# Kernel optimization log

Measured on AMD Instinct MI355X. Metric: run time of the kernel, lower is better.

Reference implementation:

```python
import jax, jax.numpy as jnp
import numpy as np

N_HEAD = 16
NEG = 1e10


def setup_inputs() -> dict:
    key = jax.random.key(0)
    k1, k2, k3 = jax.random.split(key, 3)
    nx = 1024
    B, S = 2, 2048
    x = jax.random.normal(k1, (B, S, nx), dtype=jnp.float32)
    w_attn = jax.random.normal(k2, (nx, 3 * nx), dtype=jnp.float32) * (1.0 / np.sqrt(nx))
    b_attn = jnp.zeros((3 * nx,), dtype=jnp.float32)
    w_proj = jax.random.normal(k3, (nx, nx), dtype=jnp.float32) * (1.0 / np.sqrt(nx))
    b_proj = jnp.zeros((nx,), dtype=jnp.float32)
    return {"x": x, "w_attn": w_attn, "b_attn": b_attn, "w_proj": w_proj, "b_proj": b_proj}


def reference(x, w_attn, b_attn, w_proj, b_proj):
    B, S, nx = x.shape
    d = nx // N_HEAD
    qkv = x @ w_attn + b_attn                      # [B,S,3*nx]
    q, k, v = jnp.split(qkv, 3, axis=-1)
    # split heads: [B,S,nx] -> [B,H,S,d]
    q = q.reshape(B, S, N_HEAD, d).transpose(0, 2, 1, 3)
    k = k.reshape(B, S, N_HEAD, d).transpose(0, 2, 1, 3)
    v = v.reshape(B, S, N_HEAD, d).transpose(0, 2, 1, 3)
    # present: stack of (key stored as [B,H,S,d], value) like torch code
    present = jnp.stack((k, v))                    # [2,B,H,S,d]
    # scores with scale and additive causal mask (GPT-2 style: w*b - 1e10*(1-b))
    w = jnp.einsum('bhqd,bhkd->bhqk', q, k) / jnp.sqrt(jnp.float32(d))
    mask = jnp.tril(jnp.ones((S, S), dtype=w.dtype))[None, None]
    w = w * mask - NEG * (1.0 - mask)
    w = jax.nn.softmax(w, axis=-1)
    a = jnp.einsum('bhqk,bhkd->bhqd', w, v)        # [B,H,S,d]
    a = a.transpose(0, 2, 1, 3).reshape(B, S, nx)  # merge heads
    a = a @ w_proj + b_proj
    return (a, present)
```

## Files before the change

### kernel.cpp

```cpp
#include <hip/hip_runtime.h>
#include <stdint.h>
#include <stddef.h>

#define DEVI __device__ __forceinline__

typedef __bf16 bf16x8 __attribute__((ext_vector_type(8)));
typedef float  f32x4  __attribute__((ext_vector_type(4)));
typedef float  f32x16 __attribute__((ext_vector_type(16)));
typedef unsigned short u16;
typedef uint32_t u32;
typedef u16 u16x8 __attribute__((ext_vector_type(8)));
typedef u16 u16x4 __attribute__((ext_vector_type(4)));
typedef u32 u32x2 __attribute__((ext_vector_type(2)));
typedef u32 u32x4 __attribute__((ext_vector_type(4)));

typedef __attribute__((address_space(1))) void as1_void;
typedef __attribute__((address_space(3))) void as3_void;

static constexpr float SC = 0.18033688011112042f;

DEVI u16 f2bf(float f) {
  uint32_t u = __builtin_bit_cast(uint32_t, f);
  u += 0x7fffu + ((u >> 16) & 1u);
  return (u16)(u >> 16);
}

DEVI void gload_lds16(const void* g, void* l) {
  __builtin_amdgcn_global_load_lds((as1_void*)(void*)g, (as3_void*)l, 16, 0, 0);
}

#if __has_builtin(__builtin_amdgcn_exp2f)
DEVI float fast_exp2(float x) { return __builtin_amdgcn_exp2f(x); }
#else
DEVI float fast_exp2(float x) { return exp2f(x); }
#endif

DEVI u32 cvtpk(float lo, float hi) {
  u32 r;
  asm("v_cvt_pk_bf16_f32 %0, %1, %2" : "=v"(r) : "v"(lo), "v"(hi));
  return r;
}
DEVI void plswap(u32& a, u32& b) {
  asm("v_permlane32_swap_b32 %0, %1" : "+v"(a), "+v"(b));
}

__global__ __launch_bounds__(256) void k_cvt(const float* __restrict__ in,
                                             u16* __restrict__ out, int n) {
  int i = (blockIdx.x * 256 + threadIdx.x) * 4;
  if (i >= n) return;
  const float4 v = *(const float4*)(in + i);
  u16x4 o = { f2bf(v.x), f2bf(v.y), f2bf(v.z), f2bf(v.w) };
  *(u16x4*)(out + i) = o;
}

__global__ __launch_bounds__(256) void k_tcvt(const float* __restrict__ in,
                                              u16* __restrict__ out, int R, int C) {
  __shared__ float tile[32][33];
  const int c0 = blockIdx.x * 32, r0 = blockIdx.y * 32;
  const int tx = threadIdx.x, ty = threadIdx.y;
#pragma unroll
  for (int i = ty; i < 32; i += 8)
    tile[i][tx] = in[(size_t)(r0 + i) * C + (c0 + tx)];
  __syncthreads();
#pragma unroll
  for (int i = ty; i < 32; i += 8)
    out[(size_t)(c0 + i) * R + (r0 + tx)] = f2bf(tile[tx][i]);
}

__global__ __launch_bounds__(256) void k_vt(const u16* __restrict__ in,
                                            u16* __restrict__ out) {
  __shared__ u16 tile[64][72];
  const int tid = threadIdx.x;
  const int s0 = blockIdx.x * 64;
  const int bh = blockIdx.y;
  const size_t ib = (size_t)bh * 131072;
#pragma unroll
  for (int it = 0; it < 2; ++it) {
    const int r = (tid >> 3) + it * 32;
    const int c8 = (tid & 7) * 8;
    u16x8 v = *(const u16x8*)(in + ib + (size_t)(s0 + r) * 64 + c8);
    *(u16x8*)&tile[r][c8] = v;
  }
  __syncthreads();
#pragma unroll
  for (int it = 0; it < 2; ++it) {
    const int d = (tid >> 3) + it * 32;
    const int s8 = (tid & 7) * 8;
    u16x8 v;
#pragma unroll
    for (int jj = 0; jj < 8; ++jj) v[jj] = tile[s8 + jj][d];
    *(u16x8*)(out + ib + (size_t)d * 2048 + s0 + s8) = v;
  }
}

template <int EPI>
__global__ __launch_bounds__(256) void k_gemm(
    const u16* __restrict__ A, const u16* __restrict__ Bt,
    const float* __restrict__ bias,
    u16* __restrict__ wq, u16* __restrict__ wk, u16* __restrict__ wv,
    float* __restrict__ pk, float* __restrict__ pv, float* __restrict__ of) {
  constexpr int K = 1024;
  __shared__ __align__(16) u16 Ash[2][128 * 32];
  __shared__ __align__(16) u16 Bsh[2][128 * 32];
  const int tid = threadIdx.x;
  const int lane = tid & 63, wid = tid >> 6;
  const int wm = wid >> 1, wn = wid & 1;
  const int lr = lane & 15, lg = lane >> 4;
  const int m0 = blockIdx.y * 128, n0 = blockIdx.x * 128;

  const int c = wid * 64 + lane;
  const u16* Ag1 = A + (size_t)(m0 + (c >> 2)) * K + (c & 3) * 8;
  const u16* Ag2 = A + (size_t)(m0 + 64 + (c >> 2)) * K + (c & 3) * 8;
  const u16* Bg1 = Bt + (size_t)(n0 + (c >> 2)) * K + (c & 3) * 8;
  const u16* Bg2 = Bt + (size_t)(n0 + 64 + (c >> 2)) * K + (c & 3) * 8;

  f32x4 acc[4][4];
#pragma unroll
  for (int i = 0; i < 4; ++i)
#pragma unroll
    for (int j = 0; j < 4; ++j) acc[i][j] = (f32x4)0.0f;

#define STAGE(sel, kk)                                        \
  {                                                           \
    gload_lds16(Ag1 + (kk), &Ash[sel][wid * 512]);            \
    gload_lds16(Ag2 + (kk), &Ash[sel][2048 + wid * 512]);     \
    gload_lds16(Bg1 + (kk), &Bsh[sel][wid * 512]);            \
    gload_lds16(Bg2 + (kk), &Bsh[sel][2048 + wid * 512]);     \
  }

  STAGE(0, 0)
  __syncthreads();
  int cur = 0;
  for (int k0 = 0; k0 < K; k0 += 32) {
    if (k0 + 32 < K) STAGE(cur ^ 1, k0 + 32)
    bf16x8 af[4], bfr[4];
#pragma unroll
    for (int f = 0; f < 4; ++f) {
      af[f]  = *(const bf16x8*)&Ash[cur][(wm * 64 + f * 16 + lr) * 32 + lg * 8];
      bfr[f] = *(const bf16x8*)&Bsh[cur][(wn * 64 + f * 16 + lr) * 32 + lg * 8];
    }
#pragma unroll
    for (int i = 0; i < 4; ++i)
#pragma unroll
      for (int j = 0; j < 4; ++j)
        acc[i][j] = __builtin_amdgcn_mfma_f32_16x16x32_bf16(af[i], bfr[j], acc[i][j], 0, 0, 0);
    __syncthreads();
    cur ^= 1;
  }
#undef STAGE

  if constexpr (EPI == 0) {
#pragma unroll
    for (int j = 0; j < 4; ++j) {
      const int n = n0 + wn * 64 + j * 16 + lr;
      const float bv = bias[n];
      const int sec = n >> 10;
      const int nn = n & 1023;
      const int h = nn >> 6, dd = nn & 63;
#pragma unroll
      for (int i = 0; i < 4; ++i) {
        const int mb = m0 + wm * 64 + i * 16 + lg * 4;
        const int bb = mb >> 11, ss = mb & 2047;
        const size_t ib = (size_t)(bb * 16 + h) * 131072 + (size_t)ss * 64 + dd;
        if (sec == 0) {
#pragma unroll
          for (int r = 0; r < 4; ++r)
            wq[ib + (size_t)r * 64] = f2bf(acc[i][j][r] + bv);
        } else if (sec == 1) {
#pragma unroll
          for (int r = 0; r < 4; ++r) {
            const float v = acc[i][j][r] + bv;
            wk[ib + (size_t)r * 64] = f2bf(v);
            pk[ib + (size_t)r * 64] = v;
          }
        } else {
#pragma unroll
          for (int r = 0; r < 4; ++r) {
            const float v = acc[i][j][r] + bv;
            wv[ib + (size_t)r * 64] = f2bf(v);
            pv[ib + (size_t)r * 64] = v;
          }
        }
      }
    }
  } else {
#pragma unroll
    for (int j = 0; j < 4; ++j) {
      const int n = n0 + wn * 64 + j * 16 + lr;
      const float bv = bias[n];
#pragma unroll
      for (int i = 0; i < 4; ++i) {
        const int mb = m0 + wm * 64 + i * 16 + lg * 4;
#pragma unroll
        for (int r = 0; r < 4; ++r)
          of[(size_t)(mb + r) * 1024 + n] = acc[i][j][r] + bv;
      }
    }
  }
}

__global__ __launch_bounds__(128) void k_attn(const u16* __restrict__ Q,
                                              const u16* __restrict__ Kp,
                                              const u16* __restrict__ VT,
                                              u16* __restrict__ AO) {
  __shared__ __align__(16) u16 Ksh[3][4096];
  __shared__ __align__(16) u16 Vsh[3][4096];

  const int tid = threadIdx.x;
  const int lane = tid & 63, w = tid >> 6;
  const int l31 = lane & 31, hi = lane >> 5;
  const int bid = blockIdx.x;
  const int bh = bid & 31;
  const int j4 = bid >> 8;
  const int g  = (bid >> 5) & 7;
  const int qt = (j4 == 0) ? (31 - g) : (j4 == 1) ? g : (j4 == 2) ? (23 - g) : (8 + g);
  const int b = bh >> 4, h = bh & 15;
  const size_t hb = (size_t)bh * (2048 * 64);

  const int T = qt + 1;
  const int qb = qt * 64 + w * 32;

  const int srow = w * 32 + (lane >> 3);
  const int sslot = (lane & 7) ^ (lane >> 3);
  const u16* Kg = Kp + hb + (size_t)srow * 64 + sslot * 8;
  const u16* Vg = VT + hb + (size_t)srow * 2048 + sslot * 8;

#define STAGEA(sel, jt)                                                       \
  {                                                                           \
    gload_lds16(Kg + (size_t)(jt) * 4096,          &Ksh[sel][w * 2048]);      \
    gload_lds16(Kg + (size_t)(jt) * 4096 + 512,    &Ksh[sel][w * 2048 + 512]);\
    gload_lds16(Kg + (size_t)(jt) * 4096 + 1024,   &Ksh[sel][w * 2048 + 1024]);\
    gload_lds16(Kg + (size_t)(jt) * 4096 + 1536,   &Ksh[sel][w * 2048 + 1536]);\
    gload_lds16(Vg + (size_t)(jt) * 64,            &Vsh[sel][w * 2048]);      \
    gload_lds16(Vg + (size_t)(jt) * 64 + 16384,    &Vsh[sel][w * 2048 + 512]);\
    gload_lds16(Vg + (size_t)(jt) * 64 + 32768,    &Vsh[sel][w * 2048 + 1024]);\
    gload_lds16(Vg + (size_t)(jt) * 64 + 49152,    &Vsh[sel][w * 2048 + 1536]);\
  }

  const u16* Qp = Q + hb + (size_t)(qb + l31) * 64 + hi * 8;
  const bf16x8 qf0 = *(const bf16x8*)(Qp);
  const bf16x8 qf1 = *(const bf16x8*)(Qp + 16);
  const bf16x8 qf2 = *(const bf16x8*)(Qp + 32);
  const bf16x8 qf3 = *(const bf16x8*)(Qp + 48);

  f32x16 o0 = (f32x16)0.0f, o1 = (f32x16)0.0f;
  float mrun = -1e30f, lrun = 0.0f;

  const int xr = l31 & 7;

  STAGEA(0, 0)
  if (T > 1) {
    STAGEA(1, 1)
    asm volatile("s_waitcnt vmcnt(8)" ::: "memory");
  } else {
    asm volatile("s_waitcnt vmcnt(0)" ::: "memory");
  }
  __builtin_amdgcn_sched_barrier(0);
  __builtin_amdgcn_s_barrier();
  __builtin_amdgcn_sched_barrier(0);

  int cur = 0;
  for (int jt = 0; jt < T; ++jt) {
    const bool pf = (jt + 2 < T);
    int nb = cur + 2; if (nb >= 3) nb -= 3;
    if (pf) STAGEA(nb, jt + 2)
    const u16* Kb = Ksh[cur];
    const u16* Vb = Vsh[cur];
    bf16x8 kf[2][4];
#pragma unroll
    for (int s = 0; s < 2; ++s)
#pragma unroll
      for (int c = 0; c < 4; ++c)
        kf[s][c] = *(const bf16x8*)&Kb[(s * 32 + l31) * 64 + (((2 * c + hi) ^ xr) * 8)];

    f32x16 s0 = (f32x16)0.0f, s1 = (f32x16)0.0f;
    __builtin_amdgcn_s_setprio(1);
    s0 = __builtin_amdgcn_mfma_f32_32x32x16_bf16(kf[0][0], qf0, s0, 0, 0, 0);
    s1 = __builtin_amdgcn_mfma_f32_32x32x16_bf16(kf[1][0], qf0, s1, 0, 0, 0);
    s0 = __builtin_amdgcn_mfma_f32_32x32x16_bf16(kf[0][1], qf1, s0, 0, 0, 0);
    s1 = __builtin_amdgcn_mfma_f32_32x32x16_bf16(kf[1][1], qf1, s1, 0, 0, 0);
    s0 = __builtin_amdgcn_mfma_f32_32x32x16_bf16(kf[0][2], qf2, s0, 0, 0, 0);
    s1 = __builtin_amdgcn_mfma_f32_32x32x16_bf16(kf[1][2], qf2, s1, 0, 0, 0);
    s0 = __builtin_amdgcn_mfma_f32_32x32x16_bf16(kf[0][3], qf3, s0, 0, 0, 0);
    s1 = __builtin_amdgcn_mfma_f32_32x32x16_bf16(kf[1][3], qf3, s1, 0, 0, 0);
    __builtin_amdgcn_s_setprio(0);

    if (jt == T - 1) {
      const int qrel = w * 32 + l31;
      const int h4 = hi * 4;
#pragma unroll
      for (int r = 0; r < 16; ++r) {
        const int kp = (r & 3) + ((r >> 2) << 3) + h4;
        s0[r] = (kp <= qrel) ? s0[r] : -1e30f;
        s1[r] = (kp + 32 <= qrel) ? s1[r] : -1e30f;
      }
    }

    float t8[8];
#pragma unroll
    for (int r = 0; r < 8; ++r)
      t8[r] = fmaxf(fmaxf(s0[r], s0[r + 8]), fmaxf(s1[r], s1[r + 8]));
    float tm = fmaxf(fmaxf(fmaxf(t8[0], t8[1]), fmaxf(t8[2], t8[3])),
                     fmaxf(fmaxf(t8[4], t8[5]), fmaxf(t8[6], t8[7])));
    tm = fmaxf(tm, __shfl_xor(tm, 32));
    if (!__all(tm <= mrun)) {
      const float mnew = fmaxf(mrun, tm);
      const float al = fast_exp2((mrun - mnew) * SC);
      mrun = mnew;
      lrun *= al;
#pragma unroll
      for (int r = 0; r < 16; ++r) { o0[r] *= al; o1[r] *= al; }
    }
    const float nb2 = -mrun * SC;
#pragma unroll
    for (int r = 0; r < 16; ++r) {
      s0[r] = fast_exp2(fmaf(s0[r], SC, nb2));
      s1[r] = fast_exp2(fmaf(s1[r], SC, nb2));
    }
    float u8[8];
#pragma unroll
    for (int r = 0; r < 8; ++r)
      u8[r] = (s0[r] + s0[r + 8]) + (s1[r] + s1[r + 8]);
    lrun += ((u8[0] + u8[1]) + (u8[2] + u8[3])) + ((u8[4] + u8[5]) + (u8[6] + u8[7]));

    bf16x8 pb0, pb1, pb2, pb3;
#define PACK_CHUNK(sv, bb, dst)                                   \
    {                                                             \
      u32 a0 = cvtpk(sv[bb + 0], sv[bb + 1]);                     \
      u32 a1 = cvtpk(sv[bb + 2], sv[bb + 3]);                     \
      u32 a2 = cvtpk(sv[bb + 4], sv[bb + 5]);                     \
      u32 a3 = cvtpk(sv[bb + 6], sv[bb + 7]);                     \
      plswap(a0, a2);                                             \
      plswap(a1, a3);                                             \
      u32x4 fv = {a0, a1, a2, a3};                                \
      dst = __builtin_bit_cast(bf16x8, fv);                       \
    }
    PACK_CHUNK(s0, 0, pb0)
    PACK_CHUNK(s0, 8, pb1)
    PACK_CHUNK(s1, 0, pb2)
    PACK_CHUNK(s1, 8, pb3)
#undef PACK_CHUNK

    bf16x8 vf[2][4];
#pragma unroll
    for (int mt = 0; mt < 2; ++mt)
#pragma unroll
      for (int c = 0; c < 4; ++c)
        vf[mt][c] = *(const bf16x8*)&Vb[(mt * 32 + l31) * 64 + (((2 * c + hi) ^ xr) * 8)];

    __builtin_amdgcn_s_setprio(1);
    o0 = __builtin_amdgcn_mfma_f32_32x32x16_bf16(vf[0][0], pb0, o0, 0, 0, 0);
    o1 = __builtin_amdgcn_mfma_f32_32x32x16_bf16(vf[1][0], pb0, o1, 0, 0, 0);
    o0 = __builtin_amdgcn_mfma_f32_32x32x16_bf16(vf[0][1], pb1, o0, 0, 0, 0);
    o1 = __builtin_amdgcn_mfma_f32_32x32x16_bf16(vf[1][1], pb1, o1, 0, 0, 0);
    o0 = __builtin_amdgcn_mfma_f32_32x32x16_bf16(vf[0][2], pb2, o0, 0, 0, 0);
    o1 = __builtin_amdgcn_mfma_f32_32x32x16_bf16(vf[1][2], pb2, o1, 0, 0, 0);
    o0 = __builtin_amdgcn_mfma_f32_32x32x16_bf16(vf[0][3], pb3, o0, 0, 0, 0);
    o1 = __builtin_amdgcn_mfma_f32_32x32x16_bf16(vf[1][3], pb3, o1, 0, 0, 0);
    __builtin_amdgcn_s_setprio(0);

    if (pf) asm volatile("s_waitcnt vmcnt(8)" ::: "memory");
    else    asm volatile("s_waitcnt vmcnt(0)" ::: "memory");
    __builtin_amdgcn_sched_barrier(0);
    __builtin_amdgcn_s_barrier();
    __builtin_amdgcn_sched_barrier(0);
    cur = (cur + 1 == 3) ? 0 : cur + 1;
  }
#undef STAGEA

  const float lt = lrun + __shfl_xor(lrun, 32);
  const float inv = 1.0f / lt;
  u16* aorow = AO + (size_t)(b * 2048 + qb + l31) * 1024 + h * 64 + hi * 4;
#pragma unroll
  for (int g2 = 0; g2 < 4; ++g2) {
    u32 w0 = cvtpk(o0[4 * g2 + 0] * inv, o0[4 * g2 + 1] * inv);
    u32 w1 = cvtpk(o0[4 * g2 + 2] * inv, o0[4 * g2 + 3] * inv);
    u32x2 ww = {w0, w1};
    *(u32x2*)(aorow + g2 * 8) = ww;
  }
#pragma unroll
  for (int g2 = 0; g2 < 4; ++g2) {
    u32 w0 = cvtpk(o1[4 * g2 + 0] * inv, o1[4 * g2 + 1] * inv);
    u32 w1 = cvtpk(o1[4 * g2 + 2] * inv, o1[4 * g2 + 3] * inv);
    u32x2 ww = {w0, w1};
    *(u32x2*)(aorow + 32 + g2 * 8) = ww;
  }
}

extern "C" void kernel_launch(void* const* d_in, const int* in_sizes, int n_in,
                              void* d_out, int out_size, void* d_ws, size_t ws_size,
                              hipStream_t stream) {
  const float* x      = (const float*)d_in[0];
  const float* w_attn = (const float*)d_in[1];
  const float* b_attn = (const float*)d_in[2];
  const float* w_proj = (const float*)d_in[3];
  const float* b_proj = (const float*)d_in[4];
  float* out = (float*)d_out;

  char* ws = (char*)d_ws;
  u16* x_bf  = (u16*)(ws);
  u16* wat_t = (u16*)(ws + 8388608);
  u16* wpj_t = (u16*)(ws + 14680064);
  u16* q_ws  = (u16*)(ws + 16777216);
  u16* k_ws  = (u16*)(ws + 25165824);
  u16* v_ws  = (u16*)(ws + 33554432);
  u16* a_ws  = (u16*)(ws + 41943040);
  u16* vT_ws = (u16*)(ws);

  k_cvt<<<4096, 256, 0, stream>>>(x, x_bf, 4194304);
  k_tcvt<<<dim3(96, 32), dim3(32, 8), 0, stream>>>(w_attn, wat_t, 1024, 3072);
  k_tcvt<<<dim3(32, 32), dim3(32, 8), 0, stream>>>(w_proj, wpj_t, 1024, 1024);

  k_gemm<0><<<dim3(24, 32), 256, 0, stream>>>(x_bf, wat_t, b_attn,
                                              q_ws, k_ws, v_ws,
                                              out + 4194304, out + 8388608, nullptr);

  k_vt<<<dim3(32, 32), 256, 0, stream>>>(v_ws, vT_ws);

  k_attn<<<dim3(1024), 128, 0, stream>>>(q_ws, k_ws, vT_ws, a_ws);

  k_gemm<1><<<dim3(8, 32), 256, 0, stream>>>(a_ws, wpj_t, b_proj,
                                             nullptr, nullptr, nullptr,
                                             nullptr, nullptr, out);
}
```

Measured before the change: 140.5 us.

## Triple-buffer GEMM LDS staging with explicit vmcnt waits and XCD-aware block remap

```diff
diff --git a/kernel.cpp b/kernel.cpp
--- a/kernel.cpp
+++ b/kernel.cpp
@@ -100,13 +100,19 @@
     u16* __restrict__ wq, u16* __restrict__ wk, u16* __restrict__ wv,
     float* __restrict__ pk, float* __restrict__ pv, float* __restrict__ of) {
   constexpr int K = 1024;
-  __shared__ __align__(16) u16 Ash[2][128 * 32];
-  __shared__ __align__(16) u16 Bsh[2][128 * 32];
+  constexpr int NT = K / 32;
+  __shared__ __align__(16) u16 Ash[3][128 * 32];
+  __shared__ __align__(16) u16 Bsh[3][128 * 32];
   const int tid = threadIdx.x;
   const int lane = tid & 63, wid = tid >> 6;
   const int wm = wid >> 1, wn = wid & 1;
   const int lr = lane & 15, lg = lane >> 4;
-  const int m0 = blockIdx.y * 128, n0 = blockIdx.x * 128;
+
+  const int nwgx = gridDim.x;
+  const int nwg = nwgx * gridDim.y;
+  int lbid = blockIdx.y * nwgx + blockIdx.x;
+  lbid = (lbid & 7) * (nwg >> 3) + (lbid >> 3);
+  const int m0 = (lbid / nwgx) * 128, n0 = (lbid % nwgx) * 128;
 
   const int c = wid * 64 + lane;
   const u16* Ag1 = A + (size_t)(m0 + (c >> 2)) * K + (c & 3) * 8;
@@ -129,23 +135,36 @@
   }
 
   STAGE(0, 0)
-  __syncthreads();
+  STAGE(1, 32)
+  asm volatile("s_waitcnt vmcnt(4)" ::: "memory");
+  __builtin_amdgcn_sched_barrier(0);
+  __builtin_amdgcn_s_barrier();
+  __builtin_amdgcn_sched_barrier(0);
+
   int cur = 0;
-  for (int k0 = 0; k0 < K; k0 += 32) {
-    if (k0 + 32 < K) STAGE(cur ^ 1, k0 + 32)
+  for (int j = 0; j < NT; ++j) {
+    const bool pf = (j + 2 < NT);
+    int nb = cur + 2; if (nb >= 3) nb -= 3;
+    if (pf) STAGE(nb, (j + 2) * 32)
     bf16x8 af[4], bfr[4];
 #pragma unroll
     for (int f = 0; f < 4; ++f) {
       af[f]  = *(const bf16x8*)&Ash[cur][(wm * 64 + f * 16 + lr) * 32 + lg * 8];
       bfr[f] = *(const bf16x8*)&Bsh[cur][(wn * 64 + f * 16 + lr) * 32 + lg * 8];
     }
+    __builtin_amdgcn_s_setprio(1);
 #pragma unroll
     for (int i = 0; i < 4; ++i)
 #pragma unroll
-      for (int j = 0; j < 4; ++j)
-        acc[i][j] = __builtin_amdgcn_mfma_f32_16x16x32_bf16(af[i], bfr[j], acc[i][j], 0, 0, 0);
-    __syncthreads();
-    cur ^= 1;
+      for (int jj = 0; jj < 4; ++jj)
+        acc[i][jj] = __builtin_amdgcn_mfma_f32_16x16x32_bf16(af[i], bfr[jj], acc[i][jj], 0, 0, 0);
+    __builtin_amdgcn_s_setprio(0);
+    if (pf) asm volatile("s_waitcnt vmcnt(4)" ::: "memory");
+    else    asm volatile("s_waitcnt vmcnt(0)" ::: "memory");
+    __builtin_amdgcn_sched_barrier(0);
+    __builtin_amdgcn_s_barrier();
+    __builtin_amdgcn_sched_barrier(0);
+    cur = (cur + 1 == 3) ? 0 : cur + 1;
   }
 #undef STAGE
 
```

After: 138.4 us. About the same (-1.5%).
